# Optimization experiments

Hardware: AMD Instinct MI355X
Metric: run time of the kernel (lower is better)

Reference implementation:

```python
import jax, jax.numpy as jnp
import numpy as np

EMBED_DIM = 256
NUM_HEADS = 4
HEAD_DIM = EMBED_DIM // NUM_HEADS
SCALE = HEAD_DIM ** (-0.5)


def setup_inputs() -> dict:
    key = jax.random.key(0)
    kx, kq, kp, kb = jax.random.split(key, 4)
    B, N, C = 4, 4096, EMBED_DIM
    x = jax.random.normal(kx, (B, N, C), dtype=jnp.float32)
    # qkv: Linear(C, 3C, bias=False); torch stores weight as [out, in]
    w_qkv = jax.random.normal(kq, (3 * C, C), dtype=jnp.float32) * (C ** -0.5)
    w_proj = jax.random.normal(kp, (C, C), dtype=jnp.float32) * (C ** -0.5)
    b_proj = jax.random.normal(kb, (C,), dtype=jnp.float32) * 0.01
    return {"x": x, "w_qkv": w_qkv, "w_proj": w_proj, "b_proj": b_proj}


def reference(x, w_qkv, w_proj, b_proj):
    B, N, C = x.shape
    H, D = NUM_HEADS, HEAD_DIM
    # qkv projection: [B,N,3C] -> [3,B,H,N,D]
    qkv = (x @ w_qkv.T).reshape(B, N, 3, H, D).transpose(2, 0, 3, 1, 4)
    q, k, v = qkv[0], qkv[1], qkv[2]
    # materialized [B,H,N,N] scores (faithful to the original)
    attn = jnp.einsum("bhnd,bhmd->bhnm", q, k) * SCALE
    attn_probs = jax.nn.softmax(attn, axis=-1)
    out = jnp.einsum("bhnm,bhmd->bhnd", attn_probs, v)
    out = out.transpose(0, 2, 1, 3).reshape(B, N, C)
    return out @ w_proj.T + b_proj
```

## Files before the change

kernel.cpp:

```cpp
#include <hip/hip_runtime.h>
#include <hip/hip_bf16.h>

typedef __hip_bfloat16 bf16;
typedef _Float16 f16;
typedef __attribute__((ext_vector_type(8))) short bf16x8;
typedef __attribute__((ext_vector_type(8))) _Float16 f16x8;
typedef __attribute__((ext_vector_type(2))) _Float16 f16x2;
typedef __attribute__((ext_vector_type(4))) float f32x4;
typedef __attribute__((ext_vector_type(4))) unsigned int u32x4;
typedef __attribute__((ext_vector_type(2))) unsigned int u32x2;

#define B_ 4
#define N_ 4096
#define C_ 256
#define H_ 4
#define D_ 64
#define KLN 0.18033688011112042f

#if __has_builtin(__builtin_amdgcn_exp2f)
#define EXP2(x) __builtin_amdgcn_exp2f(x)
#else
#define EXP2(x) exp2f(x)
#endif
#if __has_builtin(__builtin_amdgcn_rcpf)
#define RCP(x) __builtin_amdgcn_rcpf(x)
#else
#define RCP(x) (1.0f / (x))
#endif

__device__ inline void load_lds16(const void* g, void* l) {
#if __has_builtin(__builtin_amdgcn_global_load_lds)
    __builtin_amdgcn_global_load_lds(
        (const __attribute__((address_space(1))) unsigned int*)g,
        (__attribute__((address_space(3))) unsigned int*)l, 16, 0, 0);
#else
    int ln = __lane_id();
    ((u32x4*)l)[ln] = *((const u32x4*)g);
#endif
}

__device__ inline unsigned int pk2(float a, float b) {
    unsigned int ua = __builtin_bit_cast(unsigned int, a) + 0x8000u;
    unsigned int ub = __builtin_bit_cast(unsigned int, b) + 0x8000u;
    return (ua >> 16) | (ub & 0xffff0000u);
}
__device__ inline unsigned int pkh2(float a, float b) {
#if __has_builtin(__builtin_amdgcn_cvt_pkrtz)
    return __builtin_bit_cast(unsigned int, __builtin_amdgcn_cvt_pkrtz(a, b));
#else
    f16x2 h = { (f16)a, (f16)b };
    return __builtin_bit_cast(unsigned int, h);
#endif
}
__device__ inline short f2s(float x) {
    return (short)__builtin_bit_cast(unsigned short, __float2bfloat16(x));
}
__device__ inline bf16x8 cvt8(const float* __restrict__ p) {
    f32x4 a = *reinterpret_cast<const f32x4*>(p);
    f32x4 b = *reinterpret_cast<const f32x4*>(p + 4);
    bf16x8 r = { f2s(a[0]), f2s(a[1]), f2s(a[2]), f2s(a[3]),
                 f2s(b[0]), f2s(b[1]), f2s(b[2]), f2s(b[3]) };
    return r;
}

__global__ __launch_bounds__(256) void cast_bf16(const float* __restrict__ x,
                                                 const float* __restrict__ wq,
                                                 const float* __restrict__ wp,
                                                 bf16* __restrict__ xb,
                                                 bf16* __restrict__ wqb,
                                                 bf16* __restrict__ wpb)
{
    int bid = blockIdx.x;
    const float* s; bf16* d; int base;
    if (bid < 2048)      { s = x;  d = xb;  base = bid * 2048; }
    else if (bid < 2144) { s = wq; d = wqb; base = (bid - 2048) * 2048; }
    else                 { s = wp; d = wpb; base = (bid - 2144) * 2048; }
    int i = base + threadIdx.x * 8;
    f32x4 a = *reinterpret_cast<const f32x4*>(s + i);
    f32x4 b = *reinterpret_cast<const f32x4*>(s + i + 4);
    u32x4 o;
    o.x = pk2(a[0], a[1]); o.y = pk2(a[2], a[3]);
    o.z = pk2(b[0], b[1]); o.w = pk2(b[2], b[3]);
    *reinterpret_cast<u32x4*>(d + i) = o;
}

__global__ __launch_bounds__(256, 2) void qkv_fast(const bf16* __restrict__ x,
                                                   const bf16* __restrict__ w,
                                                   bf16* __restrict__ qw,
                                                   bf16* __restrict__ kw,
                                                   f16* __restrict__ vtw)
{
    __shared__ short w_s[64][264];
    const int tid  = threadIdx.x;
    const int lane = tid & 63;
    const int wav  = tid >> 6;
    const int quad = lane >> 4;
    const int l16  = lane & 15;
    const int mt = blockIdx.x / 12, nb = blockIdx.x % 12;
    const int m0 = mt * 64, n0 = nb * 64;

    {
        const int row = tid >> 2, cb = (tid & 3) * 64;
        const bf16* src = w + (size_t)(n0 + row) * C_ + cb;
#pragma unroll
        for (int i = 0; i < 8; ++i)
            *reinterpret_cast<bf16x8*>(&w_s[row][cb + i * 8]) =
                *reinterpret_cast<const bf16x8*>(src + i * 8);
    }
    __syncthreads();

    f32x4 acc[4] = {{0,0,0,0},{0,0,0,0},{0,0,0,0},{0,0,0,0}};
    const bf16* xrow = x + (size_t)(m0 + wav * 16 + l16) * C_ + quad * 8;
#pragma unroll
    for (int k0 = 0; k0 < C_; k0 += 32) {
        bf16x8 a = *reinterpret_cast<const bf16x8*>(xrow + k0);
#pragma unroll
        for (int nt = 0; nt < 4; ++nt) {
            bf16x8 b = *reinterpret_cast<const bf16x8*>(&w_s[nt * 16 + l16][k0 + quad * 8]);
            acc[nt] = __builtin_amdgcn_mfma_f32_16x16x32_bf16(a, b, acc[nt], 0, 0, 0);
        }
    }

    const int bb = m0 >> 12;
    const int nbase = (m0 + wav * 16) & (N_ - 1);
    if (nb < 4) {
        const int h = nb;
#pragma unroll
        for (int nt = 0; nt < 4; ++nt)
#pragma unroll
            for (int r = 0; r < 4; ++r) {
                int n = nbase + quad * 4 + r, d = nt * 16 + l16;
                qw[(((size_t)bb * H_ + h) * N_ + n) * D_ + d] =
                    __float2bfloat16(acc[nt][r] * KLN);
            }
    } else if (nb < 8) {
        const int h = nb - 4;
#pragma unroll
        for (int nt = 0; nt < 4; ++nt)
#pragma unroll
            for (int r = 0; r < 4; ++r) {
                int n = nbase + quad * 4 + r, d = nt * 16 + l16;
                kw[(((size_t)bb * H_ + h) * N_ + n) * D_ + d] =
                    __float2bfloat16(acc[nt][r]);
            }
    } else {
        const int h = nb - 8;
#pragma unroll
        for (int nt = 0; nt < 4; ++nt) {
            int d = nt * 16 + l16;
            u32x2 wv;
            wv.x = pkh2(acc[nt][0], acc[nt][1]);
            wv.y = pkh2(acc[nt][2], acc[nt][3]);
            *reinterpret_cast<u32x2*>(
                vtw + (((size_t)bb * H_ + h) * D_ + d) * N_ + nbase + quad * 4) = wv;
        }
    }
}

__global__ __launch_bounds__(256) void qkv_cvt(const float* __restrict__ x,
                                               const float* __restrict__ w,
                                               bf16* __restrict__ qw,
                                               bf16* __restrict__ kw,
                                               f16* __restrict__ vtw)
{
    const int lane = threadIdx.x & 63;
    const int wav  = threadIdx.x >> 6;
    const int quad = lane >> 4;
    const int l16  = lane & 15;
    const int gw   = blockIdx.x * 4 + wav;
    const int m0   = (gw / 12) * 16;
    const int n0   = (gw % 12) * 64;

    f32x4 acc[4] = {{0,0,0,0},{0,0,0,0},{0,0,0,0},{0,0,0,0}};
    const float* xrow = x + (size_t)(m0 + l16) * C_ + quad * 8;
#pragma unroll
    for (int k0 = 0; k0 < C_; k0 += 32) {
        bf16x8 a = cvt8(xrow + k0);
#pragma unroll
        for (int nt = 0; nt < 4; ++nt) {
            bf16x8 b = cvt8(w + (size_t)(n0 + nt * 16 + l16) * C_ + k0 + quad * 8);
            acc[nt] = __builtin_amdgcn_mfma_f32_16x16x32_bf16(a, b, acc[nt], 0, 0, 0);
        }
    }
#pragma unroll
    for (int nt = 0; nt < 4; ++nt)
#pragma unroll
        for (int r = 0; r < 4; ++r) {
            int m  = m0 + quad * 4 + r;
            int o  = n0 + nt * 16 + l16;
            int bb = m >> 12;
            int n  = m & (N_ - 1);
            if (o < 256) {
                int h = o >> 6, d = o & 63;
                qw[(((size_t)bb * H_ + h) * N_ + n) * D_ + d] =
                    __float2bfloat16(acc[nt][r] * KLN);
            } else if (o < 512) {
                int oo = o - 256; int h = oo >> 6, d = oo & 63;
                kw[(((size_t)bb * H_ + h) * N_ + n) * D_ + d] =
                    __float2bfloat16(acc[nt][r]);
            } else {
                int oo = o - 512; int h = oo >> 6, d = oo & 63;
                vtw[(((size_t)bb * H_ + h) * D_ + d) * N_ + n] = (f16)acc[nt][r];
            }
        }
}

__global__ __launch_bounds__(256, 2) void attn(const bf16* __restrict__ q,
                                               const bf16* __restrict__ k,
                                               const f16* __restrict__ vt,
                                               bf16* __restrict__ o)
{
    __shared__ short        k_s[2][64 * 64];
    __shared__ f16          v_s[2][64 * 64];
    __shared__ unsigned int p_s[4][64 * 36];

    const int tid  = threadIdx.x;
    const int lane = tid & 63;
    const int wav  = tid >> 6;
    const int quad = lane >> 4;
    const int l16  = lane & 15;
    const int l8   = l16 & 7;
    const int sub  = wav & 1;
    const int jh   = wav >> 1;
    const int bh = blockIdx.x >> 5;
    const int qt = blockIdx.x & 31;
    const int bb = bh >> 2, h = bh & 3;

    const bf16* qp = q  + (size_t)bh * N_ * D_;
    const bf16* kp = k  + (size_t)bh * N_ * D_;
    const f16*  vp = vt + (size_t)bh * D_ * N_;

    const int qbase = qt * 128 + sub * 64;
    bf16x8 qb[4][2];
#pragma unroll
    for (int qg = 0; qg < 4; ++qg)
#pragma unroll
        for (int ks = 0; ks < 2; ++ks)
            qb[qg][ks] = *reinterpret_cast<const bf16x8*>(
                qp + (size_t)(qbase + qg * 16 + l16) * D_ + ks * 32 + quad * 8);

    const int ri = lane >> 3;
    const int ci = lane & 7;
    const int gc = ci ^ ri;

    f32x4 oacc[4][4];
    f32x4 lacc[4] = {{0,0,0,0},{0,0,0,0},{0,0,0,0},{0,0,0,0}};
#pragma unroll
    for (int qg = 0; qg < 4; ++qg)
#pragma unroll
        for (int dt = 0; dt < 4; ++dt) oacc[qg][dt] = (f32x4){0,0,0,0};
    const f16x8 onesA = {1.f16, 1.f16, 1.f16, 1.f16, 1.f16, 1.f16, 1.f16, 1.f16};

    for (int t = 0; t < 32; ++t) {
        const int j0 = jh * 2048 + t * 64;
        __syncthreads();
#pragma unroll
        for (int g = 0; g < 4; ++g) {
            const int rl_ = sub * 32 + g * 8;
            load_lds16(kp + (size_t)(j0 + rl_ + ri) * D_ + gc * 8, &k_s[jh][rl_ * 64]);
            load_lds16(vp + (size_t)(rl_ + ri) * N_ + j0 + gc * 8, &v_s[jh][rl_ * 64]);
        }
        __syncthreads();

        bf16x8 ka[4][2];
#pragma unroll
        for (int nt = 0; nt < 4; ++nt)
#pragma unroll
            for (int ks = 0; ks < 2; ++ks)
                ka[nt][ks] = *reinterpret_cast<const bf16x8*>(
                    &k_s[jh][(nt * 16 + l16) * 64 + (((ks << 2) + quad) ^ l8) * 8]);

#pragma unroll
        for (int qg = 0; qg < 4; ++qg) {
            f32x4 s[4] = {{0,0,0,0},{0,0,0,0},{0,0,0,0},{0,0,0,0}};
#pragma unroll
            for (int nt = 0; nt < 4; ++nt) {
                s[nt] = __builtin_amdgcn_mfma_f32_16x16x32_bf16(ka[nt][0], qb[qg][0], s[nt], 0, 0, 0);
                s[nt] = __builtin_amdgcn_mfma_f32_16x16x32_bf16(ka[nt][1], qb[qg][1], s[nt], 0, 0, 0);
            }
            unsigned int* prow = &p_s[wav][(qg * 16 + l16) * 36];
#pragma unroll
            for (int nt = 0; nt < 4; ++nt) {
                float p0 = EXP2(s[nt][0]);
                float p1 = EXP2(s[nt][1]);
                float p2 = EXP2(s[nt][2]);
                float p3 = EXP2(s[nt][3]);
                u32x2 w2 = { pkh2(p0, p1), pkh2(p2, p3) };
                *reinterpret_cast<u32x2*>(prow + nt * 8 + quad * 2) = w2;
            }
        }
        asm volatile("" ::: "memory");

#pragma unroll
        for (int ks = 0; ks < 2; ++ks) {
            f16x8 pb[4];
#pragma unroll
            for (int qg = 0; qg < 4; ++qg) {
                u32x4 pw = *reinterpret_cast<const u32x4*>(
                    &p_s[wav][(qg * 16 + l16) * 36 + ks * 16 + quad * 4]);
                pb[qg] = __builtin_bit_cast(f16x8, pw);
                lacc[qg] = __builtin_amdgcn_mfma_f32_16x16x32_f16(onesA, pb[qg], lacc[qg], 0, 0, 0);
            }
#pragma unroll
            for (int dt = 0; dt < 4; ++dt) {
                f16x8 va = *reinterpret_cast<const f16x8*>(
                    &v_s[jh][(dt * 16 + l16) * 64 + (((ks << 2) + quad) ^ l8) * 8]);
#pragma unroll
                for (int qg = 0; qg < 4; ++qg)
                    oacc[qg][dt] = __builtin_amdgcn_mfma_f32_16x16x32_f16(va, pb[qg], oacc[qg][dt], 0, 0, 0);
            }
        }
    }

    __syncthreads();
    float* mrg = reinterpret_cast<float*>(p_s);
    if (jh == 1) {
        float* dst = mrg + (sub * 64 + lane) * 68;
#pragma unroll
        for (int qg = 0; qg < 4; ++qg) {
#pragma unroll
            for (int dt = 0; dt < 4; ++dt)
#pragma unroll
                for (int e = 0; e < 4; ++e)
                    dst[qg * 17 + dt * 4 + e] = oacc[qg][dt][e];
            dst[qg * 17 + 16] = lacc[qg][0];
        }
    }
    __syncthreads();
    if (jh == 0) {
        const float* src = mrg + (sub * 64 + lane) * 68;
#pragma unroll
        for (int qg = 0; qg < 4; ++qg) {
            float rl = RCP(lacc[qg][0] + src[qg * 17 + 16]);
            const size_t obase = ((size_t)bb * N_ + qbase + qg * 16 + l16) * C_ + h * D_;
#pragma unroll
            for (int dt = 0; dt < 4; ++dt) {
                float v0 = (oacc[qg][dt][0] + src[qg * 17 + dt * 4 + 0]) * rl;
                float v1 = (oacc[qg][dt][1] + src[qg * 17 + dt * 4 + 1]) * rl;
                float v2 = (oacc[qg][dt][2] + src[qg * 17 + dt * 4 + 2]) * rl;
                float v3 = (oacc[qg][dt][3] + src[qg * 17 + dt * 4 + 3]) * rl;
                u32x2 wv = { pk2(v0, v1), pk2(v2, v3) };
                *reinterpret_cast<u32x2*>(o + obase + dt * 16 + quad * 4) = wv;
            }
        }
    }
}

__global__ __launch_bounds__(256, 2) void out_proj_fast(const bf16* __restrict__ ov,
                                                        const bf16* __restrict__ w,
                                                        const float* __restrict__ bias,
                                                        float* __restrict__ out)
{
    __shared__ short w_s[64][264];
    const int tid  = threadIdx.x;
    const int lane = tid & 63;
    const int wav  = tid >> 6;
    const int quad = lane >> 4;
    const int l16  = lane & 15;
    const int m0 = (blockIdx.x >> 2) * 64;
    const int n0 = (blockIdx.x & 3) * 64;

    {
        const int row = tid >> 2, cb = (tid & 3) * 64;
        const bf16* src = w + (size_t)(n0 + row) * C_ + cb;
#pragma unroll
        for (int i = 0; i < 8; ++i)
            *reinterpret_cast<bf16x8*>(&w_s[row][cb + i * 8]) =
                *reinterpret_cast<const bf16x8*>(src + i * 8);
    }
    __syncthreads();

    f32x4 acc[4] = {{0,0,0,0},{0,0,0,0},{0,0,0,0},{0,0,0,0}};
    const bf16* orow = ov + (size_t)(m0 + wav * 16 + l16) * C_ + quad * 8;
#pragma unroll
    for (int k0 = 0; k0 < C_; k0 += 32) {
        bf16x8 a = *reinterpret_cast<const bf16x8*>(orow + k0);
#pragma unroll
        for (int nt = 0; nt < 4; ++nt) {
            bf16x8 b = *reinterpret_cast<const bf16x8*>(&w_s[nt * 16 + l16][k0 + quad * 8]);
            acc[nt] = __builtin_amdgcn_mfma_f32_16x16x32_bf16(a, b, acc[nt], 0, 0, 0);
        }
    }
#pragma unroll
    for (int nt = 0; nt < 4; ++nt)
#pragma unroll
        for (int r = 0; r < 4; ++r) {
            int m  = m0 + wav * 16 + quad * 4 + r;
            int oc = n0 + nt * 16 + l16;
            out[(size_t)m * C_ + oc] = acc[nt][r] + bias[oc];
        }
}

__global__ __launch_bounds__(256) void out_proj_cvt(const bf16* __restrict__ ov,
                                                    const float* __restrict__ w,
                                                    const float* __restrict__ bias,
                                                    float* __restrict__ out)
{
    const int lane = threadIdx.x & 63;
    const int wav  = threadIdx.x >> 6;
    const int quad = lane >> 4;
    const int l16  = lane & 15;
    const int gw   = blockIdx.x * 4 + wav;
    const int m0   = (gw >> 2) * 16;
    const int n0   = (gw & 3) * 64;

    f32x4 acc[4] = {{0,0,0,0},{0,0,0,0},{0,0,0,0},{0,0,0,0}};
    const bf16* orow = ov + (size_t)(m0 + l16) * C_ + quad * 8;
#pragma unroll
    for (int k0 = 0; k0 < C_; k0 += 32) {
        bf16x8 a = *reinterpret_cast<const bf16x8*>(orow + k0);
#pragma unroll
        for (int nt = 0; nt < 4; ++nt) {
            bf16x8 b = cvt8(w + (size_t)(n0 + nt * 16 + l16) * C_ + k0 + quad * 8);
            acc[nt] = __builtin_amdgcn_mfma_f32_16x16x32_bf16(a, b, acc[nt], 0, 0, 0);
        }
    }
#pragma unroll
    for (int nt = 0; nt < 4; ++nt)
#pragma unroll
        for (int r = 0; r < 4; ++r) {
            int m  = m0 + quad * 4 + r;
            int oc = n0 + nt * 16 + l16;
            out[(size_t)m * C_ + oc] = acc[nt][r] + bias[oc];
        }
}

extern "C" void kernel_launch(void* const* d_in, const int* in_sizes, int n_in,
                              void* d_out, int out_size, void* d_ws, size_t ws_size,
                              hipStream_t stream) {
    const float* x      = (const float*)d_in[0];
    const float* w_qkv  = (const float*)d_in[1];
    const float* w_proj = (const float*)d_in[2];
    const float* b_proj = (const float*)d_in[3];
    float* out = (float*)d_out;

    const size_t qkv_elems = (size_t)B_ * H_ * N_ * D_;
    bf16* q_ws  = (bf16*)d_ws;
    bf16* k_ws  = q_ws  + qkv_elems;
    f16*  vt_ws = (f16*)(k_ws + qkv_elems);
    bf16* o_ws  = (bf16*)(vt_ws + qkv_elems);
    bf16* x_bf  = o_ws  + qkv_elems;
    bf16* wq_bf = x_bf  + (size_t)B_ * N_ * C_;
    bf16* wp_bf = wq_bf + (size_t)3 * C_ * C_;

    const size_t need = ((size_t)4 * qkv_elems + (size_t)B_ * N_ * C_
                         + (size_t)3 * C_ * C_ + (size_t)C_ * C_) * 2;

    if (ws_size >= need) {
        cast_bf16    <<<2176, 256, 0, stream>>>(x, w_qkv, w_proj, x_bf, wq_bf, wp_bf);
        qkv_fast     <<<3072, 256, 0, stream>>>(x_bf, wq_bf, q_ws, k_ws, vt_ws);
        attn         <<< 512, 256, 0, stream>>>(q_ws, k_ws, vt_ws, o_ws);
        out_proj_fast<<<1024, 256, 0, stream>>>(o_ws, wp_bf, b_proj, out);
    } else {
        qkv_cvt      <<<3072, 256, 0, stream>>>(x, w_qkv, q_ws, k_ws, vt_ws);
        attn         <<< 512, 256, 0, stream>>>(q_ws, k_ws, vt_ws, o_ws);
        out_proj_cvt <<<1024, 256, 0, stream>>>(o_ws, w_proj, b_proj, out);
    }
}
```

Measured before the change: 187.8 us.

## Double-buffer attention K/V tiles, widen to 8 waves, vectorize GEMM epilogues

The attention kernel now runs 512 threads with 8 waves, each handling 32 queries. It double-buffers K/V tiles in a 64KB shared buffer so the next tile loads while the current one computes. The probabilities are kept in registers instead of going through LDS, which drops the p_s scratch and one sync per iteration. The QKV and output projection kernels swap MFMA operands so their stores become vectorized row writes, and all kernels remap block IDs so consecutive blocks are spread across XCDs. The risks are higher LDS use limiting occupancy and the K-row permutation trick needing to be exactly right.

```diff
diff --git a/kernel.cpp b/kernel.cpp
--- a/kernel.cpp
+++ b/kernel.cpp
@@ -96,7 +96,8 @@
     const int wav  = tid >> 6;
     const int quad = lane >> 4;
     const int l16  = lane & 15;
-    const int mt = blockIdx.x / 12, nb = blockIdx.x % 12;
+    const int bid = (blockIdx.x & 7) * 384 + (blockIdx.x >> 3);
+    const int mt = bid / 12, nb = bid % 12;
     const int m0 = mt * 64, n0 = nb * 64;
 
     {
@@ -111,38 +112,46 @@
 
     f32x4 acc[4] = {{0,0,0,0},{0,0,0,0},{0,0,0,0},{0,0,0,0}};
     const bf16* xrow = x + (size_t)(m0 + wav * 16 + l16) * C_ + quad * 8;
-#pragma unroll
-    for (int k0 = 0; k0 < C_; k0 += 32) {
-        bf16x8 a = *reinterpret_cast<const bf16x8*>(xrow + k0);
-#pragma unroll
-        for (int nt = 0; nt < 4; ++nt) {
-            bf16x8 b = *reinterpret_cast<const bf16x8*>(&w_s[nt * 16 + l16][k0 + quad * 8]);
-            acc[nt] = __builtin_amdgcn_mfma_f32_16x16x32_bf16(a, b, acc[nt], 0, 0, 0);
+    if (nb < 8) {
+#pragma unroll
+        for (int k0 = 0; k0 < C_; k0 += 32) {
+            bf16x8 a = *reinterpret_cast<const bf16x8*>(xrow + k0);
+#pragma unroll
+            for (int nt = 0; nt < 4; ++nt) {
+                bf16x8 b = *reinterpret_cast<const bf16x8*>(&w_s[nt * 16 + l16][k0 + quad * 8]);
+                acc[nt] = __builtin_amdgcn_mfma_f32_16x16x32_bf16(b, a, acc[nt], 0, 0, 0);
+            }
+        }
+    } else {
+#pragma unroll
+        for (int k0 = 0; k0 < C_; k0 += 32) {
+            bf16x8 a = *reinterpret_cast<const bf16x8*>(xrow + k0);
+#pragma unroll
+            for (int nt = 0; nt < 4; ++nt) {
+                bf16x8 b = *reinterpret_cast<const bf16x8*>(&w_s[nt * 16 + l16][k0 + quad * 8]);
+                acc[nt] = __builtin_amdgcn_mfma_f32_16x16x32_bf16(a, b, acc[nt], 0, 0, 0);
+            }
         }
     }
 
     const int bb = m0 >> 12;
     const int nbase = (m0 + wav * 16) & (N_ - 1);
     if (nb < 4) {
-        const int h = nb;
-#pragma unroll
-        for (int nt = 0; nt < 4; ++nt)
-#pragma unroll
-            for (int r = 0; r < 4; ++r) {
-                int n = nbase + quad * 4 + r, d = nt * 16 + l16;
-                qw[(((size_t)bb * H_ + h) * N_ + n) * D_ + d] =
-                    __float2bfloat16(acc[nt][r] * KLN);
-            }
+        bf16* dst = qw + (((size_t)bb * H_ + nb) * N_ + nbase + l16) * D_;
+#pragma unroll
+        for (int nt = 0; nt < 4; ++nt) {
+            u32x2 wv = { pk2(acc[nt][0] * KLN, acc[nt][1] * KLN),
+                         pk2(acc[nt][2] * KLN, acc[nt][3] * KLN) };
+            *reinterpret_cast<u32x2*>(dst + nt * 16 + quad * 4) = wv;
+        }
     } else if (nb < 8) {
-        const int h = nb - 4;
-#pragma unroll
-        for (int nt = 0; nt < 4; ++nt)
-#pragma unroll
-            for (int r = 0; r < 4; ++r) {
-                int n = nbase + quad * 4 + r, d = nt * 16 + l16;
-                kw[(((size_t)bb * H_ + h) * N_ + n) * D_ + d] =
-                    __float2bfloat16(acc[nt][r]);
-            }
+        bf16* dst = kw + (((size_t)bb * H_ + (nb - 4)) * N_ + nbase + l16) * D_;
+#pragma unroll
+        for (int nt = 0; nt < 4; ++nt) {
+            u32x2 wv = { pk2(acc[nt][0], acc[nt][1]),
+                         pk2(acc[nt][2], acc[nt][3]) };
+            *reinterpret_cast<u32x2*>(dst + nt * 16 + quad * 4) = wv;
+        }
     } else {
         const int h = nb - 8;
 #pragma unroll
@@ -205,35 +214,37 @@
         }
 }
 
-__global__ __launch_bounds__(256, 2) void attn(const bf16* __restrict__ q,
+__global__ __launch_bounds__(512, 4) void attn(const bf16* __restrict__ q,
                                                const bf16* __restrict__ k,
                                                const f16* __restrict__ vt,
                                                bf16* __restrict__ o)
 {
-    __shared__ short        k_s[2][64 * 64];
-    __shared__ f16          v_s[2][64 * 64];
-    __shared__ unsigned int p_s[4][64 * 36];
+    __shared__ __align__(16) char smem[65536];
+    short* k_s = reinterpret_cast<short*>(smem);
+    f16*   v_s = reinterpret_cast<f16*>(smem + 32768);
 
     const int tid  = threadIdx.x;
     const int lane = tid & 63;
     const int wav  = tid >> 6;
     const int quad = lane >> 4;
     const int l16  = lane & 15;
-    const int l8   = l16 & 7;
-    const int sub  = wav & 1;
-    const int jh   = wav >> 1;
-    const int bh = blockIdx.x >> 5;
-    const int qt = blockIdx.x & 31;
+    const int l8   = lane & 7;
+    const int sub  = wav & 3;
+    const int jh   = wav >> 2;
+
+    const int wg = (blockIdx.x & 7) * 64 + (blockIdx.x >> 3);
+    const int bh = wg >> 5;
+    const int qt = wg & 31;
     const int bb = bh >> 2, h = bh & 3;
 
     const bf16* qp = q  + (size_t)bh * N_ * D_;
     const bf16* kp = k  + (size_t)bh * N_ * D_;
     const f16*  vp = vt + (size_t)bh * D_ * N_;
 
-    const int qbase = qt * 128 + sub * 64;
-    bf16x8 qb[4][2];
-#pragma unroll
-    for (int qg = 0; qg < 4; ++qg)
+    const int qbase = qt * 128 + sub * 32;
+    bf16x8 qb[2][2];
+#pragma unroll
+    for (int qg = 0; qg < 2; ++qg)
 #pragma unroll
         for (int ks = 0; ks < 2; ++ks)
             qb[qg][ks] = *reinterpret_cast<const bf16x8*>(
@@ -242,103 +253,119 @@
     const int ri = lane >> 3;
     const int ci = lane & 7;
     const int gc = ci ^ ri;
-
-    f32x4 oacc[4][4];
-    f32x4 lacc[4] = {{0,0,0,0},{0,0,0,0},{0,0,0,0},{0,0,0,0}};
-#pragma unroll
-    for (int qg = 0; qg < 4; ++qg)
-#pragma unroll
-        for (int dt = 0; dt < 4; ++dt) oacc[qg][dt] = (f32x4){0,0,0,0};
+    int koff[2], voff[2], lds_r[2];
+#pragma unroll
+    for (int g = 0; g < 2; ++g) {
+        const int rb  = sub * 16 + g * 8;
+        const int rho = rb + ri;
+        const int pr  = (rho & 32) | ((rho & 12) << 1) | ((rho & 16) >> 2) | (rho & 3);
+        koff[g]  = pr * D_ + gc * 8;
+        voff[g]  = rho * N_ + gc * 8;
+        lds_r[g] = rb * 64;
+    }
+
+    f32x4 oacc[2][4];
+    f32x4 lacc[2];
+#pragma unroll
+    for (int qg = 0; qg < 2; ++qg) {
+        lacc[qg] = (f32x4){0, 0, 0, 0};
+#pragma unroll
+        for (int dt = 0; dt < 4; ++dt) oacc[qg][dt] = (f32x4){0, 0, 0, 0};
+    }
     const f16x8 onesA = {1.f16, 1.f16, 1.f16, 1.f16, 1.f16, 1.f16, 1.f16, 1.f16};
 
+    auto stage = [&](int buf, int t) {
+        const int j0 = jh * 2048 + t * 64;
+        short* kd = k_s + (size_t)(buf * 2 + jh) * 4096;
+        f16*   vd = v_s + (size_t)(buf * 2 + jh) * 4096;
+#pragma unroll
+        for (int g = 0; g < 2; ++g) {
+            load_lds16(kp + (size_t)j0 * D_ + koff[g], kd + lds_r[g]);
+            load_lds16(vp + j0 + voff[g],              vd + lds_r[g]);
+        }
+    };
+
+    stage(0, 0);
+    __syncthreads();
+
     for (int t = 0; t < 32; ++t) {
-        const int j0 = jh * 2048 + t * 64;
-        __syncthreads();
-#pragma unroll
-        for (int g = 0; g < 4; ++g) {
-            const int rl_ = sub * 32 + g * 8;
-            load_lds16(kp + (size_t)(j0 + rl_ + ri) * D_ + gc * 8, &k_s[jh][rl_ * 64]);
-            load_lds16(vp + (size_t)(rl_ + ri) * N_ + j0 + gc * 8, &v_s[jh][rl_ * 64]);
-        }
-        __syncthreads();
-
-        bf16x8 ka[4][2];
-#pragma unroll
-        for (int nt = 0; nt < 4; ++nt)
-#pragma unroll
-            for (int ks = 0; ks < 2; ++ks)
-                ka[nt][ks] = *reinterpret_cast<const bf16x8*>(
-                    &k_s[jh][(nt * 16 + l16) * 64 + (((ks << 2) + quad) ^ l8) * 8]);
-
-#pragma unroll
-        for (int qg = 0; qg < 4; ++qg) {
-            f32x4 s[4] = {{0,0,0,0},{0,0,0,0},{0,0,0,0},{0,0,0,0}};
-#pragma unroll
-            for (int nt = 0; nt < 4; ++nt) {
-                s[nt] = __builtin_amdgcn_mfma_f32_16x16x32_bf16(ka[nt][0], qb[qg][0], s[nt], 0, 0, 0);
-                s[nt] = __builtin_amdgcn_mfma_f32_16x16x32_bf16(ka[nt][1], qb[qg][1], s[nt], 0, 0, 0);
-            }
-            unsigned int* prow = &p_s[wav][(qg * 16 + l16) * 36];
-#pragma unroll
-            for (int nt = 0; nt < 4; ++nt) {
-                float p0 = EXP2(s[nt][0]);
-                float p1 = EXP2(s[nt][1]);
-                float p2 = EXP2(s[nt][2]);
-                float p3 = EXP2(s[nt][3]);
-                u32x2 w2 = { pkh2(p0, p1), pkh2(p2, p3) };
-                *reinterpret_cast<u32x2*>(prow + nt * 8 + quad * 2) = w2;
-            }
-        }
-        asm volatile("" ::: "memory");
-
-#pragma unroll
-        for (int ks = 0; ks < 2; ++ks) {
-            f16x8 pb[4];
-#pragma unroll
-            for (int qg = 0; qg < 4; ++qg) {
-                u32x4 pw = *reinterpret_cast<const u32x4*>(
-                    &p_s[wav][(qg * 16 + l16) * 36 + ks * 16 + quad * 4]);
-                pb[qg] = __builtin_bit_cast(f16x8, pw);
-                lacc[qg] = __builtin_amdgcn_mfma_f32_16x16x32_f16(onesA, pb[qg], lacc[qg], 0, 0, 0);
-            }
+        const int cur = t & 1;
+        if (t < 31) stage(cur ^ 1, t + 1);
+
+        const short* kt  = k_s + (size_t)(cur * 2 + jh) * 4096;
+        const f16*   vtl = v_s + (size_t)(cur * 2 + jh) * 4096;
+
+        f32x4 s[2][4];
+#pragma unroll
+        for (int qg = 0; qg < 2; ++qg)
+#pragma unroll
+            for (int nt = 0; nt < 4; ++nt) s[qg][nt] = (f32x4){0, 0, 0, 0};
+#pragma unroll
+        for (int nt = 0; nt < 4; ++nt) {
+            const int rb = (nt * 16 + l16) * 64;
+            bf16x8 k0 = *reinterpret_cast<const bf16x8*>(kt + rb + ((quad    ) ^ l8) * 8);
+            bf16x8 k1 = *reinterpret_cast<const bf16x8*>(kt + rb + ((4 + quad) ^ l8) * 8);
+#pragma unroll
+            for (int qg = 0; qg < 2; ++qg) {
+                s[qg][nt] = __builtin_amdgcn_mfma_f32_16x16x32_bf16(k0, qb[qg][0], s[qg][nt], 0, 0, 0);
+                s[qg][nt] = __builtin_amdgcn_mfma_f32_16x16x32_bf16(k1, qb[qg][1], s[qg][nt], 0, 0, 0);
+            }
+        }
+
+        f16x8 pb[2][2];
+#pragma unroll
+        for (int qg = 0; qg < 2; ++qg)
+#pragma unroll
+            for (int ks = 0; ks < 2; ++ks) {
+                const f32x4 sa = s[qg][2 * ks], sb = s[qg][2 * ks + 1];
+                u32x4 pw;
+                pw.x = pkh2(EXP2(sa[0]), EXP2(sa[1]));
+                pw.y = pkh2(EXP2(sa[2]), EXP2(sa[3]));
+                pw.z = pkh2(EXP2(sb[0]), EXP2(sb[1]));
+                pw.w = pkh2(EXP2(sb[2]), EXP2(sb[3]));
+                pb[qg][ks] = __builtin_bit_cast(f16x8, pw);
+                lacc[qg] = __builtin_amdgcn_mfma_f32_16x16x32_f16(onesA, pb[qg][ks], lacc[qg], 0, 0, 0);
+            }
+
+#pragma unroll
+        for (int ks = 0; ks < 2; ++ks)
 #pragma unroll
             for (int dt = 0; dt < 4; ++dt) {
                 f16x8 va = *reinterpret_cast<const f16x8*>(
-                    &v_s[jh][(dt * 16 + l16) * 64 + (((ks << 2) + quad) ^ l8) * 8]);
-#pragma unroll
-                for (int qg = 0; qg < 4; ++qg)
-                    oacc[qg][dt] = __builtin_amdgcn_mfma_f32_16x16x32_f16(va, pb[qg], oacc[qg][dt], 0, 0, 0);
-            }
-        }
-    }
-
-    __syncthreads();
-    float* mrg = reinterpret_cast<float*>(p_s);
+                    vtl + (dt * 16 + l16) * 64 + (((ks << 2) + quad) ^ l8) * 8);
+#pragma unroll
+                for (int qg = 0; qg < 2; ++qg)
+                    oacc[qg][dt] = __builtin_amdgcn_mfma_f32_16x16x32_f16(va, pb[qg][ks], oacc[qg][dt], 0, 0, 0);
+            }
+
+        __syncthreads();
+    }
+
+    float* mrg = reinterpret_cast<float*>(smem);
+    const int slot = (sub * 64 + lane) * 35;
     if (jh == 1) {
-        float* dst = mrg + (sub * 64 + lane) * 68;
-#pragma unroll
-        for (int qg = 0; qg < 4; ++qg) {
+#pragma unroll
+        for (int qg = 0; qg < 2; ++qg) {
 #pragma unroll
             for (int dt = 0; dt < 4; ++dt)
 #pragma unroll
                 for (int e = 0; e < 4; ++e)
-                    dst[qg * 17 + dt * 4 + e] = oacc[qg][dt][e];
-            dst[qg * 17 + 16] = lacc[qg][0];
+                    mrg[slot + qg * 17 + dt * 4 + e] = oacc[qg][dt][e];
+            mrg[slot + qg * 17 + 16] = lacc[qg][0];
         }
     }
     __syncthreads();
     if (jh == 0) {
-        const float* src = mrg + (sub * 64 + lane) * 68;
-#pragma unroll
-        for (int qg = 0; qg < 4; ++qg) {
-            float rl = RCP(lacc[qg][0] + src[qg * 17 + 16]);
+#pragma unroll
+        for (int qg = 0; qg < 2; ++qg) {
+            const float rl = RCP(lacc[qg][0] + mrg[slot + qg * 17 + 16]);
             const size_t obase = ((size_t)bb * N_ + qbase + qg * 16 + l16) * C_ + h * D_;
 #pragma unroll
             for (int dt = 0; dt < 4; ++dt) {
-                float v0 = (oacc[qg][dt][0] + src[qg * 17 + dt * 4 + 0]) * rl;
-                float v1 = (oacc[qg][dt][1] + src[qg * 17 + dt * 4 + 1]) * rl;
-                float v2 = (oacc[qg][dt][2] + src[qg * 17 + dt * 4 + 2]) * rl;
-                float v3 = (oacc[qg][dt][3] + src[qg * 17 + dt * 4 + 3]) * rl;
+                float v0 = (oacc[qg][dt][0] + mrg[slot + qg * 17 + dt * 4 + 0]) * rl;
+                float v1 = (oacc[qg][dt][1] + mrg[slot + qg * 17 + dt * 4 + 1]) * rl;
+                float v2 = (oacc[qg][dt][2] + mrg[slot + qg * 17 + dt * 4 + 2]) * rl;
+                float v3 = (oacc[qg][dt][3] + mrg[slot + qg * 17 + dt * 4 + 3]) * rl;
                 u32x2 wv = { pk2(v0, v1), pk2(v2, v3) };
                 *reinterpret_cast<u32x2*>(o + obase + dt * 16 + quad * 4) = wv;
             }
@@ -357,8 +384,9 @@
     const int wav  = tid >> 6;
     const int quad = lane >> 4;
     const int l16  = lane & 15;
-    const int m0 = (blockIdx.x >> 2) * 64;
-    const int n0 = (blockIdx.x & 3) * 64;
+    const int bid = (blockIdx.x & 7) * 128 + (blockIdx.x >> 3);
+    const int m0 = (bid >> 2) * 64;
+    const int n0 = (bid & 3) * 64;
 
     {
         const int row = tid >> 2, cb = (tid & 3) * 64;
@@ -378,17 +406,17 @@
 #pragma unroll
         for (int nt = 0; nt < 4; ++nt) {
             bf16x8 b = *reinterpret_cast<const bf16x8*>(&w_s[nt * 16 + l16][k0 + quad * 8]);
-            acc[nt] = __builtin_amdgcn_mfma_f32_16x16x32_bf16(a, b, acc[nt], 0, 0, 0);
-        }
-    }
-#pragma unroll
-    for (int nt = 0; nt < 4; ++nt)
-#pragma unroll
-        for (int r = 0; r < 4; ++r) {
-            int m  = m0 + wav * 16 + quad * 4 + r;
-            int oc = n0 + nt * 16 + l16;
-            out[(size_t)m * C_ + oc] = acc[nt][r] + bias[oc];
-        }
+            acc[nt] = __builtin_amdgcn_mfma_f32_16x16x32_bf16(b, a, acc[nt], 0, 0, 0);
+        }
+    }
+    const int m = m0 + wav * 16 + l16;
+#pragma unroll
+    for (int nt = 0; nt < 4; ++nt) {
+        const int oc0 = n0 + nt * 16 + quad * 4;
+        f32x4 bv = *reinterpret_cast<const f32x4*>(bias + oc0);
+        f32x4 ovv = acc[nt] + bv;
+        *reinterpret_cast<f32x4*>(out + (size_t)m * C_ + oc0) = ovv;
+    }
 }
 
 __global__ __launch_bounds__(256) void out_proj_cvt(const bf16* __restrict__ ov,
@@ -449,11 +477,11 @@
     if (ws_size >= need) {
         cast_bf16    <<<2176, 256, 0, stream>>>(x, w_qkv, w_proj, x_bf, wq_bf, wp_bf);
         qkv_fast     <<<3072, 256, 0, stream>>>(x_bf, wq_bf, q_ws, k_ws, vt_ws);
-        attn         <<< 512, 256, 0, stream>>>(q_ws, k_ws, vt_ws, o_ws);
+        attn         <<< 512, 512, 0, stream>>>(q_ws, k_ws, vt_ws, o_ws);
         out_proj_fast<<<1024, 256, 0, stream>>>(o_ws, wp_bf, b_proj, out);
     } else {
         qkv_cvt      <<<3072, 256, 0, stream>>>(x, w_qkv, q_ws, k_ws, vt_ws);
-        attn         <<< 512, 256, 0, stream>>>(q_ws, k_ws, vt_ws, o_ws);
+        attn         <<< 512, 512, 0, stream>>>(q_ws, k_ws, vt_ws, o_ws);
         out_proj_cvt <<<1024, 256, 0, stream>>>(o_ws, w_proj, b_proj, out);
     }
 }
```

After: 181.9 us. 1.03x faster.
